# Optimization experiments

Hardware: AMD Instinct MI355X
Metric: run time of the kernel (lower is better)

## Reference

```python
import jax, jax.numpy as jnp
import numpy as np

DIM = 768
NUM_HEADS = 12
HEAD_DIM = DIM // NUM_HEADS
SCALE = HEAD_DIM ** -0.5
B, N = 4, 2048


def setup_inputs() -> dict:
    key = jax.random.key(0)
    k1, k2, k3 = jax.random.split(key, 3)
    x = jax.random.normal(k1, (B, N, DIM), dtype=jnp.float32)
    W_qk = jax.random.normal(k2, (2 * DIM, DIM), dtype=jnp.float32) * (DIM ** -0.5)
    b_qk = jax.random.normal(k3, (2 * DIM,), dtype=jnp.float32) * 0.02
    return {"x": x, "W_qk": W_qk, "b_qk": b_qk}


def reference(x, W_qk, b_qk):
    Bb, Nn, C = x.shape
    # qk projection: [B,N,2C] -> [B,N,2,H,D] -> q,k each [B,H,N,D]
    qk = x @ W_qk.T + b_qk
    qk = qk.reshape(Bb, Nn, 2, NUM_HEADS, HEAD_DIM).transpose(2, 0, 3, 1, 4)
    q, k = qk[0], qk[1]
    # attention scores [B,H,N,N]
    attn = jnp.einsum("bhnd,bhmd->bhnm", q, k) * SCALE
    attn = jax.nn.softmax(attn, axis=-1)
    # mean over heads, then per-query diagonal -> [B,N]
    attn_weights = jnp.diagonal(attn.mean(axis=1), axis1=-2, axis2=-1)
    return attn_weights
```

## Files before the change

kernel.cpp:

```cpp
#include <hip/hip_runtime.h>
#include <math.h>


#define B_ 4
#define N_ 2048
#define H_ 12
#define D_ 64
#define C_ 768
#define TWO_C 1536
#define QSCALE 0.18033688011112043f

typedef _Float16 half8 __attribute__((ext_vector_type(8)));
typedef _Float16 half4 __attribute__((ext_vector_type(4)));
typedef float floatx4 __attribute__((ext_vector_type(4)));

#if __has_builtin(__builtin_amdgcn_exp2f)
#define EXP2(x) __builtin_amdgcn_exp2f(x)
#else
#define EXP2(x) exp2f(x)
#endif

__device__ __forceinline__ void gload_lds16(const _Float16* g, _Float16* l) {
  __builtin_amdgcn_global_load_lds(
      (const __attribute__((address_space(1))) void*)g,
      (__attribute__((address_space(3))) void*)l, 16, 0, 0);
}

__global__ __launch_bounds__(256) void conv_kernel(const float* __restrict__ in,
                                                   _Float16* __restrict__ out,
                                                   int n4) {
  int i = blockIdx.x * 256 + threadIdx.x;
  if (i >= n4) return;
  float4 v = ((const float4*)in)[i];
  half4 o;
  o[0] = (_Float16)v.x; o[1] = (_Float16)v.y;
  o[2] = (_Float16)v.z; o[3] = (_Float16)v.w;
  ((half4*)out)[i] = o;
}

__global__ __launch_bounds__(256) void proj_kernel(
    const _Float16* __restrict__ xh, const _Float16* __restrict__ wh,
    const float* __restrict__ bias, _Float16* __restrict__ qh,
    _Float16* __restrict__ kh) {
  __shared__ _Float16 As[128 * 32];
  __shared__ _Float16 Bs[128 * 32];
  const int t = threadIdx.x;
  const int l = t & 63;
  const int w = t >> 6;
  const int wr = w >> 1, wc = w & 1;

  int lin = blockIdx.y * 12 + blockIdx.x;
  int swz = (lin & 7) * 96 + (lin >> 3);
  const int bm = (swz / 12) * 128;
  const int bc = (swz % 12) * 128;

  const int srow = l >> 2;
  const int schunk = (l & 3) ^ ((l >> 3) & 3);

  floatx4 acc[4][4] = {};

  for (int k0 = 0; k0 < C_; k0 += 32) {
    __syncthreads();
#pragma unroll
    for (int i = 0; i < 2; ++i) {
      int rbase = w * 32 + i * 16;
      const _Float16* ga =
          xh + (size_t)(bm + rbase + srow) * C_ + k0 + schunk * 8;
      gload_lds16(ga, As + rbase * 32);
      const _Float16* gb =
          wh + (size_t)(bc + rbase + srow) * C_ + k0 + schunk * 8;
      gload_lds16(gb, Bs + rbase * 32);
    }
    __syncthreads();

    half8 af[4], bf[4];
#pragma unroll
    for (int fr = 0; fr < 4; ++fr) {
      int row = wr * 64 + fr * 16 + (l & 15);
      int ch = (l >> 4) ^ ((row >> 1) & 3);
      af[fr] = *(const half8*)(As + row * 32 + ch * 8);
    }
#pragma unroll
    for (int fc = 0; fc < 4; ++fc) {
      int row = wc * 64 + fc * 16 + (l & 15);
      int ch = (l >> 4) ^ ((row >> 1) & 3);
      bf[fc] = *(const half8*)(Bs + row * 32 + ch * 8);
    }
#pragma unroll
    for (int fr = 0; fr < 4; ++fr)
#pragma unroll
      for (int fc = 0; fc < 4; ++fc)
        acc[fr][fc] = __builtin_amdgcn_mfma_f32_16x16x32_f16(
            af[fr], bf[fc], acc[fr][fc], 0, 0, 0);
  }

#pragma unroll
  for (int fr = 0; fr < 4; ++fr) {
#pragma unroll
    for (int fc = 0; fc < 4; ++fc) {
#pragma unroll
      for (int j = 0; j < 4; ++j) {
        int m = bm + wr * 64 + fr * 16 + ((l >> 4) << 2) + j;
        int c = bc + wc * 64 + fc * 16 + (l & 15);
        float v = acc[fr][fc][j] + bias[c];
        int b = m >> 11, n = m & (N_ - 1);
        int cc = (c < C_) ? c : c - C_;
        if (c < C_) v *= QSCALE;
        int hh = cc >> 6, d = cc & 63;
        _Float16* dst = (c < C_) ? qh : kh;
        dst[((((size_t)b * H_ + hh) * N_ + n) << 6) + d] = (_Float16)v;
      }
    }
  }
}

__global__ __launch_bounds__(256) void attn_kernel(
    const _Float16* __restrict__ qh, const _Float16* __restrict__ kh,
    float* __restrict__ part) {
  __shared__ _Float16 ks[2][64 * 64];
  const int t = threadIdx.x;
  const int l = t & 63;
  const int w = t >> 6;

  int lin = blockIdx.x;
  int swz = (lin & 7) * 192 + (lin >> 3);
  const int qt = swz & 31;
  const int h = (swz >> 5) % 12;
  const int b = swz / 384;

  const _Float16* qb = qh + (((size_t)(b * H_ + h) * N_ + qt * 64) << 6);
  const _Float16* kb = kh + (((size_t)(b * H_ + h) * N_) << 6);

  half8 qf[4][2];
#pragma unroll
  for (int fr = 0; fr < 4; ++fr)
#pragma unroll
    for (int kd = 0; kd < 2; ++kd)
      qf[fr][kd] = *(const half8*)(qb + (size_t)(fr * 16 + (l & 15)) * 64 +
                                   kd * 32 + (l >> 4) * 8);

  const int lin0 = w * 64 + l;
  const int row0 = lin0 >> 3, slot0 = lin0 & 7;
  const int soff0 = row0 * 64 + (slot0 ^ (row0 & 7)) * 8;
  const int lin1 = lin0 + 256;
  const int row1 = lin1 >> 3, slot1 = lin1 & 7;
  const int soff1 = row1 * 64 + (slot1 ^ (row1 & 7)) * 8;

#define STAGE(BUF, KT)                                         \
  {                                                            \
    const _Float16* kp_ = kb + (size_t)(KT) * 4096;            \
    gload_lds16(kp_ + soff0, &ks[BUF][(w * 64) * 8]);          \
    gload_lds16(kp_ + soff1, &ks[BUF][(w * 64 + 256) * 8]);    \
  }

  const int frow = w * 16 + (l & 15);
  const int koff0 = frow * 64 + (((l >> 4) + 0) ^ (l & 7)) * 8;
  const int koff1 = frow * 64 + (((l >> 4) + 4) ^ (l & 7)) * 8;

  float lsum[4][4] = {};
  float ed[4] = {0.f, 0.f, 0.f, 0.f};

  STAGE(0, 0);
  __syncthreads();

  int buf = 0;
  for (int kt = 0; kt < 32; ++kt) {
    if (kt + 1 < 32) STAGE(buf ^ 1, kt + 1);

    half8 kf0 = *(const half8*)&ks[buf][koff0];
    half8 kf1 = *(const half8*)&ks[buf][koff1];

    floatx4 acc[4] = {};
#pragma unroll
    for (int fr = 0; fr < 4; ++fr) {
      acc[fr] =
          __builtin_amdgcn_mfma_f32_16x16x32_f16(qf[fr][0], kf0, acc[fr], 0, 0, 0);
      acc[fr] =
          __builtin_amdgcn_mfma_f32_16x16x32_f16(qf[fr][1], kf1, acc[fr], 0, 0, 0);
    }

#pragma unroll
    for (int fr = 0; fr < 4; ++fr)
#pragma unroll
      for (int j = 0; j < 4; ++j) {
        float e = EXP2(acc[fr][j]);
        lsum[fr][j] += e;
        if (kt == qt && fr == w && (l & 15) == (((l >> 4) << 2) + j)) ed[j] = e;
      }

    __syncthreads();
    buf ^= 1;
  }
#undef STAGE

#pragma unroll
  for (int fr = 0; fr < 4; ++fr)
#pragma unroll
    for (int j = 0; j < 4; ++j)
#pragma unroll
      for (int m = 1; m < 16; m <<= 1)
        lsum[fr][j] += __shfl_xor(lsum[fr][j], m, 16);
#pragma unroll
  for (int j = 0; j < 4; ++j)
#pragma unroll
    for (int m = 1; m < 16; m <<= 1) ed[j] += __shfl_xor(ed[j], m, 16);

  float* red = (float*)ks;
  float* edl = red + 256;
  if ((l & 15) == 0) {
#pragma unroll
    for (int fr = 0; fr < 4; ++fr)
#pragma unroll
      for (int j = 0; j < 4; ++j)
        red[w * 64 + fr * 16 + ((l >> 4) << 2) + j] = lsum[fr][j];
#pragma unroll
    for (int j = 0; j < 4; ++j) edl[w * 16 + ((l >> 4) << 2) + j] = ed[j];
  }
  __syncthreads();

  if (t < 64) {
    float ls = red[t] + red[64 + t] + red[128 + t] + red[192 + t];
    part[(size_t)(b * H_ + h) * N_ + qt * 64 + t] = edl[t] / ls;
  }
}

__global__ __launch_bounds__(256) void reduce_kernel(
    const float* __restrict__ part, float* __restrict__ out) {
  int g = blockIdx.x * 256 + threadIdx.x;
  if (g >= B_ * N_) return;
  int b = g >> 11, n = g & (N_ - 1);
  float s = 0.0f;
#pragma unroll
  for (int hh = 0; hh < H_; ++hh) s += part[(size_t)(b * H_ + hh) * N_ + n];
  out[g] = s * (1.0f / (float)H_);
}

extern "C" void kernel_launch(void* const* d_in, const int* in_sizes, int n_in,
                              void* d_out, int out_size, void* d_ws,
                              size_t ws_size, hipStream_t stream) {
  const float* x = (const float*)d_in[0];
  const float* W = (const float*)d_in[1];
  const float* bias = (const float*)d_in[2];
  float* out = (float*)d_out;

  char* ws = (char*)d_ws;
  _Float16* xh = (_Float16*)ws;
  _Float16* wh = (_Float16*)(ws + 12582912);
  _Float16* qh = (_Float16*)(ws + 14942208);
  _Float16* kh = (_Float16*)(ws + 27525120);
  float* part = (float*)(ws + 40108032);

  conv_kernel<<<(1572864 + 255) / 256, 256, 0, stream>>>(x, xh, 1572864);
  conv_kernel<<<(294912 + 255) / 256, 256, 0, stream>>>(W, wh, 294912);
  proj_kernel<<<dim3(TWO_C / 128, 8192 / 128), 256, 0, stream>>>(xh, wh, bias,
                                                                 qh, kh);
  attn_kernel<<<N_ / 64 * H_ * B_, 256, 0, stream>>>(qh, kh, part);
  reduce_kernel<<<(B_ * N_ + 255) / 256, 256, 0, stream>>>(part, out);
}
```

Before: 91.30 us.

## Load K fragments directly to registers and merge conversion launches

The attention kernel stops staging K tiles through double-buffered shared memory with per-iteration barriers. Each wave now loads its own K fragments straight from global memory into registers, using a two-deep software prefetch and no __syncthreads in the loop. The two fp32-to-fp16 conversion launches are merged into one kernel. This removes barrier and LDS traffic and one launch, but each wave now reads K with a less coalesced pattern and depends on cache hits.

```diff
diff --git a/kernel.cpp b/kernel.cpp
--- a/kernel.cpp
+++ b/kernel.cpp
@@ -26,16 +26,28 @@
       (__attribute__((address_space(3))) void*)l, 16, 0, 0);
 }
 
-__global__ __launch_bounds__(256) void conv_kernel(const float* __restrict__ in,
-                                                   _Float16* __restrict__ out,
-                                                   int n4) {
+#define NX4 1572864
+#define NW4 294912
+__global__ __launch_bounds__(256) void conv_kernel(const float* __restrict__ x,
+                                                   const float* __restrict__ W,
+                                                   _Float16* __restrict__ xh,
+                                                   _Float16* __restrict__ wh) {
   int i = blockIdx.x * 256 + threadIdx.x;
-  if (i >= n4) return;
-  float4 v = ((const float4*)in)[i];
+  const float* in;
+  _Float16* out;
+  int idx;
+  if (i < NX4) {
+    in = x; out = xh; idx = i;
+  } else if (i < NX4 + NW4) {
+    in = W; out = wh; idx = i - NX4;
+  } else {
+    return;
+  }
+  float4 v = ((const float4*)in)[idx];
   half4 o;
   o[0] = (_Float16)v.x; o[1] = (_Float16)v.y;
   o[2] = (_Float16)v.z; o[3] = (_Float16)v.w;
-  ((half4*)out)[i] = o;
+  ((half4*)out)[idx] = o;
 }
 
 __global__ __launch_bounds__(256) void proj_kernel(
@@ -117,7 +129,7 @@
 __global__ __launch_bounds__(256) void attn_kernel(
     const _Float16* __restrict__ qh, const _Float16* __restrict__ kh,
     float* __restrict__ part) {
-  __shared__ _Float16 ks[2][64 * 64];
+  __shared__ float red[5 * 64];
   const int t = threadIdx.x;
   const int l = t & 63;
   const int w = t >> 6;
@@ -139,59 +151,46 @@
       qf[fr][kd] = *(const half8*)(qb + (size_t)(fr * 16 + (l & 15)) * 64 +
                                    kd * 32 + (l >> 4) * 8);
 
-  const int lin0 = w * 64 + l;
-  const int row0 = lin0 >> 3, slot0 = lin0 & 7;
-  const int soff0 = row0 * 64 + (slot0 ^ (row0 & 7)) * 8;
-  const int lin1 = lin0 + 256;
-  const int row1 = lin1 >> 3, slot1 = lin1 & 7;
-  const int soff1 = row1 * 64 + (slot1 ^ (row1 & 7)) * 8;
-
-#define STAGE(BUF, KT)                                         \
-  {                                                            \
-    const _Float16* kp_ = kb + (size_t)(KT) * 4096;            \
-    gload_lds16(kp_ + soff0, &ks[BUF][(w * 64) * 8]);          \
-    gload_lds16(kp_ + soff1, &ks[BUF][(w * 64 + 256) * 8]);    \
-  }
-
-  const int frow = w * 16 + (l & 15);
-  const int koff0 = frow * 64 + (((l >> 4) + 0) ^ (l & 7)) * 8;
-  const int koff1 = frow * 64 + (((l >> 4) + 4) ^ (l & 7)) * 8;
+  const _Float16* kl = kb + (w * 16 + (l & 15)) * 64 + (l >> 4) * 8;
 
   float lsum[4][4] = {};
   float ed[4] = {0.f, 0.f, 0.f, 0.f};
 
-  STAGE(0, 0);
-  __syncthreads();
-
-  int buf = 0;
-  for (int kt = 0; kt < 32; ++kt) {
-    if (kt + 1 < 32) STAGE(buf ^ 1, kt + 1);
-
-    half8 kf0 = *(const half8*)&ks[buf][koff0];
-    half8 kf1 = *(const half8*)&ks[buf][koff1];
-
-    floatx4 acc[4] = {};
-#pragma unroll
-    for (int fr = 0; fr < 4; ++fr) {
-      acc[fr] =
-          __builtin_amdgcn_mfma_f32_16x16x32_f16(qf[fr][0], kf0, acc[fr], 0, 0, 0);
-      acc[fr] =
-          __builtin_amdgcn_mfma_f32_16x16x32_f16(qf[fr][1], kf1, acc[fr], 0, 0, 0);
-    }
-
-#pragma unroll
-    for (int fr = 0; fr < 4; ++fr)
-#pragma unroll
-      for (int j = 0; j < 4; ++j) {
-        float e = EXP2(acc[fr][j]);
-        lsum[fr][j] += e;
-        if (kt == qt && fr == w && (l & 15) == (((l >> 4) << 2) + j)) ed[j] = e;
-      }
-
-    __syncthreads();
-    buf ^= 1;
-  }
-#undef STAGE
+#define LOADK(KT, K0, K1)                                      \
+  {                                                            \
+    const _Float16* p_ = kl + (size_t)((KT) & 31) * 4096;      \
+    K0 = *(const half8*)p_;                                    \
+    K1 = *(const half8*)(p_ + 32);                             \
+  }
+
+#define COMPUTE(KT, K0, K1)                                                   \
+  {                                                                           \
+    floatx4 acc[4] = {};                                                      \
+    _Pragma("unroll") for (int fr = 0; fr < 4; ++fr) {                        \
+      acc[fr] = __builtin_amdgcn_mfma_f32_16x16x32_f16(qf[fr][0], K0,         \
+                                                       acc[fr], 0, 0, 0);     \
+      acc[fr] = __builtin_amdgcn_mfma_f32_16x16x32_f16(qf[fr][1], K1,         \
+                                                       acc[fr], 0, 0, 0);     \
+    }                                                                         \
+    _Pragma("unroll") for (int fr = 0; fr < 4; ++fr)                          \
+        _Pragma("unroll") for (int j = 0; j < 4; ++j) {                       \
+      float e = EXP2(acc[fr][j]);                                             \
+      lsum[fr][j] += e;                                                       \
+      if ((KT) == qt && fr == w && (l & 15) == (((l >> 4) << 2) + j))         \
+        ed[j] = e;                                                            \
+    }                                                                         \
+  }
+
+  half8 a0, a1, b0, b1;
+  LOADK(0, a0, a1);
+  for (int kt = 0; kt < 32; kt += 2) {
+    LOADK(kt + 1, b0, b1);
+    COMPUTE(kt, a0, a1);
+    LOADK(kt + 2, a0, a1);
+    COMPUTE(kt + 1, b0, b1);
+  }
+#undef LOADK
+#undef COMPUTE
 
 #pragma unroll
   for (int fr = 0; fr < 4; ++fr)
@@ -205,7 +204,6 @@
 #pragma unroll
     for (int m = 1; m < 16; m <<= 1) ed[j] += __shfl_xor(ed[j], m, 16);
 
-  float* red = (float*)ks;
   float* edl = red + 256;
   if ((l & 15) == 0) {
 #pragma unroll
@@ -250,8 +248,7 @@
   _Float16* kh = (_Float16*)(ws + 27525120);
   float* part = (float*)(ws + 40108032);
 
-  conv_kernel<<<(1572864 + 255) / 256, 256, 0, stream>>>(x, xh, 1572864);
-  conv_kernel<<<(294912 + 255) / 256, 256, 0, stream>>>(W, wh, 294912);
+  conv_kernel<<<(NX4 + NW4 + 255) / 256, 256, 0, stream>>>(x, W, xh, wh);
   proj_kernel<<<dim3(TWO_C / 128, 8192 / 128), 256, 0, stream>>>(xh, wh, bias,
                                                                  qh, kh);
   attn_kernel<<<N_ / 64 * H_ * B_, 256, 0, stream>>>(qh, kh, part);
```

Measured after the change: 100.2 us. 1.1x slower.
